# Kernel optimization log

Measured on AMD Instinct MI355X. Metric: run time of the kernel, lower is better.

## Reference

```python
import jax, jax.numpy as jnp
import numpy as np

H = 64  # hidden size


def _gru_cell(x, h, Wih, Whh, bih, bhh):
    """PyTorch-convention GRU cell. x:[B,in], h:[B,H]. Gate order: r, z, n."""
    gi = x @ Wih.T + bih              # [B, 3H]
    gh = h @ Whh.T + bhh              # [B, 3H]
    ir, iz, in_ = jnp.split(gi, 3, axis=-1)
    hr, hz, hn = jnp.split(gh, 3, axis=-1)
    r = jax.nn.sigmoid(ir + hr)
    z = jax.nn.sigmoid(iz + hz)
    n = jnp.tanh(in_ + r * hn)
    return (1.0 - z) * n + z * h


def setup_inputs() -> dict:
    key = jax.random.key(0)
    B, T, NIN = 4096, 256, 6
    ks = jax.random.split(key, 24)

    def w(k, shape, fan):
        return (jax.random.normal(k, shape, jnp.float32) / np.sqrt(fan).astype(np.float32))

    inp = {"x": jax.random.normal(ks[0], (B, T, NIN), jnp.float32)}
    # encoder layer 0 (input 6) and layer 1 (input 64)
    inp["enc_Wih0"] = w(ks[1], (3 * H, NIN), H)
    inp["enc_Whh0"] = w(ks[2], (3 * H, H), H)
    inp["enc_bih0"] = w(ks[3], (3 * H,), H)
    inp["enc_bhh0"] = w(ks[4], (3 * H,), H)
    inp["enc_Wih1"] = w(ks[5], (3 * H, H), H)
    inp["enc_Whh1"] = w(ks[6], (3 * H, H), H)
    inp["enc_bih1"] = w(ks[7], (3 * H,), H)
    inp["enc_bhh1"] = w(ks[8], (3 * H,), H)
    # decoder layer 0 (input 1) and layer 1 (input 64)
    inp["dec_Wih0"] = w(ks[9], (3 * H, 1), H)
    inp["dec_Whh0"] = w(ks[10], (3 * H, H), H)
    inp["dec_bih0"] = w(ks[11], (3 * H,), H)
    inp["dec_bhh0"] = w(ks[12], (3 * H,), H)
    inp["dec_Wih1"] = w(ks[13], (3 * H, H), H)
    inp["dec_Whh1"] = w(ks[14], (3 * H, H), H)
    inp["dec_bih1"] = w(ks[15], (3 * H,), H)
    inp["dec_bhh1"] = w(ks[16], (3 * H,), H)
    # output head
    inp["out_W"] = w(ks[17], (1, H), H)
    inp["out_b"] = w(ks[18], (1,), H)
    inp["target_len"] = 180
    return inp


def reference(x, enc_Wih0, enc_Whh0, enc_bih0, enc_bhh0,
              enc_Wih1, enc_Whh1, enc_bih1, enc_bhh1,
              dec_Wih0, dec_Whh0, dec_bih0, dec_bhh0,
              dec_Wih1, dec_Whh1, dec_bih1, dec_bhh1,
              out_W, out_b, target_len):
    B = x.shape[0]
    dtype = x.dtype

    # ---- encoder: 2-layer GRU over x, return final hidden per layer ----
    seq = jnp.swapaxes(x, 0, 1)  # [T, B, 6] time-major
    enc_layers = [(enc_Wih0, enc_Whh0, enc_bih0, enc_bhh0),
                  (enc_Wih1, enc_Whh1, enc_bih1, enc_bhh1)]
    h_finals = []
    for (Wih, Whh, bih, bhh) in enc_layers:
        def step(h, xt, Wih=Wih, Whh=Whh, bih=bih, bhh=bhh):
            hn = _gru_cell(xt, h, Wih, Whh, bih, bhh)
            return hn, hn
        h_last, seq = jax.lax.scan(step, jnp.zeros((B, H), dtype), seq)
        h_finals.append(h_last)

    def dec_step(carry, _):
        h0, h1, prev = carry
        h0 = _gru_cell(prev, h0, dec_Wih0, dec_Whh0, dec_bih0, dec_bhh0)
        h1 = _gru_cell(h0, h1, dec_Wih1, dec_Whh1, dec_bih1, dec_bhh1)
        cv = h1 @ out_W.T + out_b  # [B, 1]
        return (h0, h1, cv), cv

    prev0 = jnp.zeros((B, 1), dtype)
    _, outs = jax.lax.scan(dec_step, (h_finals[0], h_finals[1], prev0),
                           None, length=target_len)
    return jnp.swapaxes(outs, 0, 1)  # [B, target_len, 1]
```

## Files before the change

kernel.cpp:

```cpp
#include <hip/hip_runtime.h>
#include <cstdint>

typedef _Float16 half8 __attribute__((ext_vector_type(8)));
typedef __attribute__((ext_vector_type(4))) float floatx4;

#define TSEQ 256
#define TDEC 180
#define NIN  6
#define GROWS 16
#define NBLK (4096 / GROWS)
#define NSL 4
#define RS0 104
#define RS1 72
#define L2E 1.4426950408889634f

__device__ __forceinline__ floatx4 mfma16(half8 a, half8 b, floatx4 c) {
  return __builtin_amdgcn_mfma_f32_16x16x32_f16(a, b, c, 0, 0, 0);
}

__device__ __forceinline__ void sigm2pair(float vr, float vz, float& gr, float& gz) {
  const float d1 = 1.0f + __builtin_amdgcn_exp2f(-vr);
  const float d2 = 1.0f + __builtin_amdgcn_exp2f(-vz);
  const float rp = __builtin_amdgcn_rcpf(d1 * d2);
  gr = rp * d2;
  gz = rp * d1;
}
__device__ __forceinline__ float tanh2(float v) {
  return fmaf(2.0f, __builtin_amdgcn_rcpf(1.0f + __builtin_amdgcn_exp2f(-v)), -1.0f);
}

__device__ __forceinline__ half8 ldh8(const _Float16* p) { return *(const half8*)p; }

#define PASS2_I3(F0, F1, r, z, g, W, QR, QZ, QG) do {                   \
  r = mfma16(F0, W[0][0], QR); z = mfma16(F0, W[1][0], QZ); g = mfma16(F0, W[2][0], QG); \
  r = mfma16(F1, W[0][1], r);  z = mfma16(F1, W[1][1], z);  g = mfma16(F1, W[2][1], g);  \
} while (0)

#define PASS2_A2I1(F0, F1, r, z, g, W, QG) do {                         \
  r = mfma16(F0, W[0][0], r); z = mfma16(F0, W[1][0], z); g = mfma16(F0, W[2][0], QG); \
  r = mfma16(F1, W[0][1], r); z = mfma16(F1, W[1][1], z); g = mfma16(F1, W[2][1], g);  \
} while (0)

#define PASS1_A2I1(F0, r, z, g, W, QG) do {                             \
  r = mfma16(F0, W[0][0], r); z = mfma16(F0, W[1][0], z); g = mfma16(F0, W[2][0], QG); \
} while (0)

#define SYNC() do {                                         \
  asm volatile("s_waitcnt lgkmcnt(0)" ::: "memory");        \
  __builtin_amdgcn_s_barrier();                             \
  asm volatile("" ::: "memory");                            \
} while (0)

__global__ void __launch_bounds__(512, 2)
gru_persist(const float* __restrict__ x,
            const float* __restrict__ eWih0, const float* __restrict__ eWhh0,
            const float* __restrict__ ebih0, const float* __restrict__ ebhh0,
            const float* __restrict__ eWih1, const float* __restrict__ eWhh1,
            const float* __restrict__ ebih1, const float* __restrict__ ebhh1,
            const float* __restrict__ dWih0, const float* __restrict__ dWhh0,
            const float* __restrict__ dbih0, const float* __restrict__ dbhh0,
            const float* __restrict__ dWih1, const float* __restrict__ dWhh1,
            const float* __restrict__ dbih1, const float* __restrict__ dbhh1,
            const float* __restrict__ outW, const float* __restrict__ outB,
            float* __restrict__ out)
{
  __shared__ __align__(16) _Float16 s0[NSL][16][RS0];
  __shared__ __align__(16) _Float16 s1[NSL][16][RS1];

  const int tid  = threadIdx.x;
  const bool isA = tid < 256;
  const int wvL  = (tid >> 6) & 3;
  const int lane = tid & 63;
  const int c    = lane & 15;
  const int q    = lane >> 4;
  const int u    = wvL * 16 + c;
  const long base = (long)blockIdx.x * GROWS;

  for (int i = tid; i < NSL * 16 * RS0; i += 512) ((uint16_t*)s0)[i] = 0;
  for (int i = tid; i < NSL * 16 * RS1; i += 512) ((uint16_t*)s1)[i] = 0;
  if (tid < GROWS * NIN) {
    int m = tid / 6, i2 = tid - m * 6;
    s0[0][m][64 + i2] = (_Float16)x[(base + m) * (TSEQ * NIN) + i2];
  }

  half8 W1[3][2], W2[3][2];
  half8 W1d[3][2], W2d[3][2];
  float hr[4] = {0, 0, 0, 0};
  const float SC[3] = {L2E, L2E, 2.0f * L2E};

  auto loadW64 = [&](const float* W, half8 (&D)[3][2]) {
    #pragma unroll
    for (int s = 0; s < 3; s++) {
      const int n = (s * 4 + wvL) * 16 + c;
      #pragma unroll
      for (int kt = 0; kt < 2; kt++) {
        const int k0 = kt * 32 + q * 8;
        #pragma unroll
        for (int j = 0; j < 8; j++) D[s][kt][j] = (_Float16)(SC[s] * W[n * 64 + k0 + j]);
      }
    }
  };

  const float ob = outB[0];
  float cR, cZ, c3, c4;
  float dR, dZ, d3, d4;
  float bR0 = 0, bZ0 = 0, b30 = 0, b40 = 0;
  float wk[2][8];
  if (isA) {
    loadW64(eWhh0, W1);
    #pragma unroll
    for (int s = 0; s < 3; s++) {
      const int n = (s * 4 + wvL) * 16 + c;
      #pragma unroll
      for (int kt = 0; kt < 2; kt++)
        #pragma unroll
        for (int j = 0; j < 8; j++) {
          float v = (kt == 0 && q == 0 && j < NIN) ? SC[s] * eWih0[n * NIN + j] : 0.0f;
          W2[s][kt][j] = (_Float16)v;
        }
    }
    loadW64(dWhh0, W1d);
    #pragma unroll
    for (int s = 0; s < 3; s++) {
      const int n = (s * 4 + wvL) * 16 + c;
      const float wd = SC[s] * dWih0[n];
      #pragma unroll
      for (int kt = 0; kt < 2; kt++) {
        const int k0 = kt * 32 + q * 8;
        #pragma unroll
        for (int j = 0; j < 8; j++) W2d[s][kt][j] = (_Float16)(wd * outW[k0 + j]);
      }
    }
    cR = L2E * (ebih0[u] + ebhh0[u]);
    cZ = L2E * (ebih0[64 + u] + ebhh0[64 + u]);
    c3 = 2.0f * L2E * ebhh0[128 + u];
    c4 = 2.0f * L2E * ebih0[128 + u];
    bR0 = L2E * (dbih0[u] + dbhh0[u]);
    bZ0 = L2E * (dbih0[64 + u] + dbhh0[64 + u]);
    b30 = 2.0f * L2E * dbhh0[128 + u];
    b40 = 2.0f * L2E * dbih0[128 + u];
    dR = bR0 + L2E * (dWih0[u] * ob);
    dZ = bZ0 + L2E * (dWih0[64 + u] * ob);
    d3 = b30;
    d4 = b40 + 2.0f * L2E * (dWih0[128 + u] * ob);
  } else {
    loadW64(eWih1, W1); loadW64(eWhh1, W2);
    loadW64(dWih1, W1d); loadW64(dWhh1, W2d);
    cR = L2E * (ebih1[u] + ebhh1[u]);
    cZ = L2E * (ebih1[64 + u] + ebhh1[64 + u]);
    c3 = 2.0f * L2E * ebih1[128 + u];
    c4 = 2.0f * L2E * ebhh1[128 + u];
    dR = L2E * (dbih1[u] + dbhh1[u]);
    dZ = L2E * (dbih1[64 + u] + dbhh1[64 + u]);
    d3 = 2.0f * L2E * dbih1[128 + u];
    d4 = 2.0f * L2E * dbhh1[128 + u];
    #pragma unroll
    for (int kt = 0; kt < 2; kt++)
      #pragma unroll
      for (int j = 0; j < 8; j++) wk[kt][j] = outW[kt * 32 + q * 8 + j];
  }
  __syncthreads();

  if (isA) {
    floatx4 QR = {cR, cR, cR, cR}, QZ = {cZ, cZ, cZ, cZ};
    floatx4 Q3 = {c3, c3, c3, c3}, Q4 = {c4, c4, c4, c4};
    const bool doX = (lane < 24);
    const float *px0 = nullptr;
    int xo0 = 0;
    float xa0 = 0.f, xb0 = 0.f;
    if (doX) {
      int s_ = wvL * 24 + lane;
      int m0 = s_ / 6, i0 = s_ - m0 * 6;
      px0 = x + (base + m0) * (TSEQ * NIN) + i0;
      xo0 = m0 * RS0 + 64 + i0;
      xa0 = px0[NIN];
      xb0 = px0[2 * NIN];
    }
    for (int k = 0; k < TSEQ; k += 4) {
      #pragma unroll
      for (int h4 = 0; h4 < 4; h4++) {
        const int i_ = k + h4, p = h4, pn = (h4 + 1) & 3;
        const half8 a0 = ldh8(&s0[p][c][q * 8]);
        const half8 a1 = ldh8(&s0[p][c][32 + q * 8]);
        const half8 xf = ldh8(&s0[p][c][64 + q * 8]);
        floatx4 aR, aZ, a3, a4;
        PASS2_I3(a0, a1, aR, aZ, a3, W1, QR, QZ, Q3);
        PASS1_A2I1(xf, aR, aZ, a4, W2, Q4);
        if (doX && i_ + 1 < TSEQ) {
          ((_Float16*)s0[pn])[xo0] = (_Float16)xa0;
          xa0 = xb0;
          if (i_ + 3 < TSEQ) xb0 = px0[(i_ + 3) * NIN];
        }
        #pragma unroll
        for (int r4 = 0; r4 < 4; r4++) {
          float gr, gz;
          sigm2pair(aR[r4], aZ[r4], gr, gz);
          const float nn = tanh2(a4[r4] + gr * a3[r4]);
          const float hn = nn + gz * (hr[r4] - nn);
          hr[r4] = hn;
          s0[pn][q * 4 + r4][u] = (_Float16)hn;
        }
        SYNC();
      }
    }
    {
      const half8 a0 = ldh8(&s0[0][c][q * 8]);
      const half8 a1 = ldh8(&s0[0][c][32 + q * 8]);
      const floatx4 TR = {bR0, bR0, bR0, bR0}, TZ = {bZ0, bZ0, bZ0, bZ0};
      const floatx4 T3 = {b30, b30, b30, b30};
      floatx4 aR, aZ, a3;
      floatx4 a4 = {b40, b40, b40, b40};
      PASS2_I3(a0, a1, aR, aZ, a3, W1d, TR, TZ, T3);
      #pragma unroll
      for (int r4 = 0; r4 < 4; r4++) {
        float gr, gz;
        sigm2pair(aR[r4], aZ[r4], gr, gz);
        const float nn = tanh2(a4[r4] + gr * a3[r4]);
        const float hn = nn + gz * (hr[r4] - nn);
        hr[r4] = hn;
        s0[1][q * 4 + r4][u] = (_Float16)hn;
      }
      SYNC();
    }
    QR = (floatx4){dR, dR, dR, dR}; QZ = (floatx4){dZ, dZ, dZ, dZ};
    Q3 = (floatx4){d3, d3, d3, d3}; Q4 = (floatx4){d4, d4, d4, d4};
    for (int i_ = TSEQ + 1; i_ < TSEQ + TDEC; i_++) {
      const int p = i_ & 3, pn = (i_ + 1) & 3;
      const half8 a0 = ldh8(&s0[p][c][q * 8]);
      const half8 a1 = ldh8(&s0[p][c][32 + q * 8]);
      floatx4 aR, aZ, a3, a4;
      PASS2_I3(a0, a1, aR, aZ, a3, W1d, QR, QZ, Q3);
      SYNC();
      const half8 b0 = ldh8(&s1[p][c][q * 8]);
      const half8 b1 = ldh8(&s1[p][c][32 + q * 8]);
      PASS2_A2I1(b0, b1, aR, aZ, a4, W2d, Q4);
      #pragma unroll
      for (int r4 = 0; r4 < 4; r4++) {
        float gr, gz;
        sigm2pair(aR[r4], aZ[r4], gr, gz);
        const float nn = tanh2(a4[r4] + gr * a3[r4]);
        const float hn = nn + gz * (hr[r4] - nn);
        hr[r4] = hn;
        s0[pn][q * 4 + r4][u] = (_Float16)hn;
      }
      SYNC();
    }
    SYNC();
  } else {
    floatx4 QR = {cR, cR, cR, cR}, QZ = {cZ, cZ, cZ, cZ};
    floatx4 Q3 = {c3, c3, c3, c3}, Q4 = {c4, c4, c4, c4};
    for (int k = 0; k < TSEQ; k += 4) {
      #pragma unroll
      for (int h4 = 0; h4 < 4; h4++) {
        const int kk = k + h4;
        if (kk > 0) {
          const int p = (h4 + 3) & 3, pn = h4;
          const half8 f0 = ldh8(&s1[p][c][q * 8]);
          const half8 f1 = ldh8(&s1[p][c][32 + q * 8]);
          floatx4 aR, aZ, a3, a4;
          PASS2_I3(f0, f1, aR, aZ, a4, W2, QR, QZ, Q4);
          const half8 g0 = ldh8(&s0[pn][c][q * 8]);
          const half8 g1 = ldh8(&s0[pn][c][32 + q * 8]);
          PASS2_A2I1(g0, g1, aR, aZ, a3, W1, Q3);
          #pragma unroll
          for (int r4 = 0; r4 < 4; r4++) {
            float gr, gz;
            sigm2pair(aR[r4], aZ[r4], gr, gz);
            const float nn = tanh2(a3[r4] + gr * a4[r4]);
            const float hn = nn + gz * (hr[r4] - nn);
            hr[r4] = hn;
            s1[pn][q * 4 + r4][u] = (_Float16)hn;
          }
        }
        SYNC();
      }
    }
    {
      const half8 f0 = ldh8(&s1[3][c][q * 8]);
      const half8 f1 = ldh8(&s1[3][c][32 + q * 8]);
      floatx4 aR, aZ, a3, a4;
      PASS2_I3(f0, f1, aR, aZ, a4, W2, QR, QZ, Q4);
      const half8 g0 = ldh8(&s0[0][c][q * 8]);
      const half8 g1 = ldh8(&s0[0][c][32 + q * 8]);
      PASS2_A2I1(g0, g1, aR, aZ, a3, W1, Q3);
      #pragma unroll
      for (int r4 = 0; r4 < 4; r4++) {
        float gr, gz;
        sigm2pair(aR[r4], aZ[r4], gr, gz);
        const float nn = tanh2(a3[r4] + gr * a4[r4]);
        const float hn = nn + gz * (hr[r4] - nn);
        hr[r4] = hn;
        s1[0][q * 4 + r4][u] = (_Float16)hn;
      }
      SYNC();
    }
    QR = (floatx4){dR, dR, dR, dR}; QZ = (floatx4){dZ, dZ, dZ, dZ};
    Q3 = (floatx4){d3, d3, d3, d3}; Q4 = (floatx4){d4, d4, d4, d4};
    {
      const half8 f0 = ldh8(&s1[0][c][q * 8]);
      const half8 f1 = ldh8(&s1[0][c][32 + q * 8]);
      floatx4 aR, aZ, a3, a4;
      PASS2_I3(f0, f1, aR, aZ, a4, W2d, QR, QZ, Q4);
      const half8 g0 = ldh8(&s0[1][c][q * 8]);
      const half8 g1 = ldh8(&s0[1][c][32 + q * 8]);
      PASS2_A2I1(g0, g1, aR, aZ, a3, W1d, Q3);
      #pragma unroll
      for (int r4 = 0; r4 < 4; r4++) {
        float gr, gz;
        sigm2pair(aR[r4], aZ[r4], gr, gz);
        const float nn = tanh2(a3[r4] + gr * a4[r4]);
        const float hn = nn + gz * (hr[r4] - nn);
        hr[r4] = hn;
        s1[1][q * 4 + r4][u] = (_Float16)hn;
      }
      SYNC();
    }
    for (int i_ = TSEQ + 1; i_ < TSEQ + TDEC; i_++) {
      const int p = i_ & 3, pn = (i_ + 1) & 3;
      const half8 f0 = ldh8(&s1[p][c][q * 8]);
      const half8 f1 = ldh8(&s1[p][c][32 + q * 8]);
      floatx4 aR, aZ, a3, a4;
      PASS2_I3(f0, f1, aR, aZ, a4, W2d, QR, QZ, Q4);
      if (wvL == 0) {
        float cv = 0.0f;
        #pragma unroll
        for (int j = 0; j < 8; j++) {
          cv = fmaf((float)f0[j], wk[0][j], cv);
          cv = fmaf((float)f1[j], wk[1][j], cv);
        }
        cv += __shfl_xor(cv, 16);
        cv += __shfl_xor(cv, 32);
        if (lane < 16) out[(base + lane) * TDEC + (i_ - TSEQ - 1)] = cv + ob;
      }
      SYNC();
      const half8 g0 = ldh8(&s0[pn][c][q * 8]);
      const half8 g1 = ldh8(&s0[pn][c][32 + q * 8]);
      PASS2_A2I1(g0, g1, aR, aZ, a3, W1d, Q3);
      #pragma unroll
      for (int r4 = 0; r4 < 4; r4++) {
        float gr, gz;
        sigm2pair(aR[r4], aZ[r4], gr, gz);
        const float nn = tanh2(a3[r4] + gr * a4[r4]);
        const float hn = nn + gz * (hr[r4] - nn);
        hr[r4] = hn;
        s1[pn][q * 4 + r4][u] = (_Float16)hn;
      }
      SYNC();
    }
    if (wvL == 0) {
      const half8 f0 = ldh8(&s1[0][c][q * 8]);
      const half8 f1 = ldh8(&s1[0][c][32 + q * 8]);
      float cv = 0.0f;
      #pragma unroll
      for (int j = 0; j < 8; j++) {
        cv = fmaf((float)f0[j], wk[0][j], cv);
        cv = fmaf((float)f1[j], wk[1][j], cv);
      }
      cv += __shfl_xor(cv, 16);
      cv += __shfl_xor(cv, 32);
      if (lane < 16) out[(base + lane) * TDEC + (TDEC - 1)] = cv + ob;
    }
  }
}

extern "C" void kernel_launch(void* const* d_in, const int* in_sizes, int n_in,
                              void* d_out, int out_size, void* d_ws, size_t ws_size,
                              hipStream_t stream) {
  (void)in_sizes; (void)n_in; (void)d_ws; (void)ws_size; (void)out_size;
  const float* x     = (const float*)d_in[0];
  const float* eWih0 = (const float*)d_in[1];
  const float* eWhh0 = (const float*)d_in[2];
  const float* ebih0 = (const float*)d_in[3];
  const float* ebhh0 = (const float*)d_in[4];
  const float* eWih1 = (const float*)d_in[5];
  const float* eWhh1 = (const float*)d_in[6];
  const float* ebih1 = (const float*)d_in[7];
  const float* ebhh1 = (const float*)d_in[8];
  const float* dWih0 = (const float*)d_in[9];
  const float* dWhh0 = (const float*)d_in[10];
  const float* dbih0 = (const float*)d_in[11];
  const float* dbhh0 = (const float*)d_in[12];
  const float* dWih1 = (const float*)d_in[13];
  const float* dWhh1 = (const float*)d_in[14];
  const float* dbih1 = (const float*)d_in[15];
  const float* dbhh1 = (const float*)d_in[16];
  const float* outW  = (const float*)d_in[17];
  const float* outB  = (const float*)d_in[18];
  hipLaunchKernelGGL(gru_persist, dim3(NBLK), dim3(512), 0, stream,
                     x, eWih0, eWhh0, ebih0, ebhh0, eWih1, eWhh1, ebih1, ebhh1,
                     dWih0, dWhh0, dbih0, dbhh0, dWih1, dWhh1, dbih1, dbhh1,
                     outW, outB, (float*)d_out);
}
```

Measured before the change: 362.9 us.

## Merge two GRU layer wave groups into single 256-thread block per row tile

Replaces the 512-thread block, where the first 256 threads ran layer 0 and the second 256 ran layer 1, with 256 threads that each compute both layers in the same step. The encoder pipelines layer 1 for step i-1 alongside layer 0 for step i inside one barrier interval. Decoder weights are loaded after the encoder finishes to limit register pressure. Launch bounds change to (256,1); this halves the threads working on each tile and roughly doubles the serial MFMA and transcendental work per wave, in exchange for less cross-group synchronisation.

```diff
diff --git a/kernel.cpp b/kernel.cpp
--- a/kernel.cpp
+++ b/kernel.cpp
@@ -14,6 +14,7 @@
 #define RS1 72
 #define L2E 1.4426950408889634f
 
+
 __device__ __forceinline__ floatx4 mfma16(half8 a, half8 b, floatx4 c) {
   return __builtin_amdgcn_mfma_f32_16x16x32_f16(a, b, c, 0, 0, 0);
 }
@@ -30,6 +31,7 @@
 }
 
 __device__ __forceinline__ half8 ldh8(const _Float16* p) { return *(const half8*)p; }
+__device__ __forceinline__ floatx4 sp4(float v) { return (floatx4){v, v, v, v}; }
 
 #define PASS2_I3(F0, F1, r, z, g, W, QR, QZ, QG) do {                   \
   r = mfma16(F0, W[0][0], QR); z = mfma16(F0, W[1][0], QZ); g = mfma16(F0, W[2][0], QG); \
@@ -41,8 +43,8 @@
   r = mfma16(F1, W[0][1], r); z = mfma16(F1, W[1][1], z); g = mfma16(F1, W[2][1], g);  \
 } while (0)
 
-#define PASS1_A2I1(F0, r, z, g, W, QG) do {                             \
-  r = mfma16(F0, W[0][0], r); z = mfma16(F0, W[1][0], z); g = mfma16(F0, W[2][0], QG); \
+#define PASS1_I1(F0, r, z, g, W3, QG) do {                              \
+  r = mfma16(F0, W3[0], r); z = mfma16(F0, W3[1], z); g = mfma16(F0, W3[2], QG); \
 } while (0)
 
 #define SYNC() do {                                         \
@@ -51,7 +53,7 @@
   asm volatile("" ::: "memory");                            \
 } while (0)
 
-__global__ void __launch_bounds__(512, 2)
+__global__ void __launch_bounds__(256, 1)
 gru_persist(const float* __restrict__ x,
             const float* __restrict__ eWih0, const float* __restrict__ eWhh0,
             const float* __restrict__ ebih0, const float* __restrict__ ebhh0,
@@ -68,24 +70,26 @@
   __shared__ __align__(16) _Float16 s1[NSL][16][RS1];
 
   const int tid  = threadIdx.x;
-  const bool isA = tid < 256;
-  const int wvL  = (tid >> 6) & 3;
+  const int wvL  = tid >> 6;
   const int lane = tid & 63;
   const int c    = lane & 15;
   const int q    = lane >> 4;
   const int u    = wvL * 16 + c;
   const long base = (long)blockIdx.x * GROWS;
 
-  for (int i = tid; i < NSL * 16 * RS0; i += 512) ((uint16_t*)s0)[i] = 0;
-  for (int i = tid; i < NSL * 16 * RS1; i += 512) ((uint16_t*)s1)[i] = 0;
+  for (int i = tid; i < NSL * 16 * RS0; i += 256) ((uint16_t*)s0)[i] = 0;
+  for (int i = tid; i < NSL * 16 * RS1; i += 256) ((uint16_t*)s1)[i] = 0;
   if (tid < GROWS * NIN) {
     int m = tid / 6, i2 = tid - m * 6;
     s0[0][m][64 + i2] = (_Float16)x[(base + m) * (TSEQ * NIN) + i2];
   }
 
-  half8 W1[3][2], W2[3][2];
-  half8 W1d[3][2], W2d[3][2];
-  float hr[4] = {0, 0, 0, 0};
+  half8 W1[3][2];
+  half8 W2e[3];
+  half8 W1B[3][2];
+  half8 W2B[3][2];
+  float hr0[4] = {0, 0, 0, 0};
+  float hr1[4] = {0, 0, 0, 0};
   const float SC[3] = {L2E, L2E, 2.0f * L2E};
 
   auto loadW64 = [&](const float* W, half8 (&D)[3][2]) {
@@ -101,265 +105,241 @@
     }
   };
 
+  loadW64(eWhh0, W1);
+  #pragma unroll
+  for (int s = 0; s < 3; s++) {
+    const int n = (s * 4 + wvL) * 16 + c;
+    #pragma unroll
+    for (int j = 0; j < 8; j++) {
+      float v = (q == 0 && j < NIN) ? SC[s] * eWih0[n * NIN + j] : 0.0f;
+      W2e[s][j] = (_Float16)v;
+    }
+  }
+  loadW64(eWih1, W1B);
+  loadW64(eWhh1, W2B);
+
   const float ob = outB[0];
-  float cR, cZ, c3, c4;
-  float dR, dZ, d3, d4;
-  float bR0 = 0, bZ0 = 0, b30 = 0, b40 = 0;
   float wk[2][8];
-  if (isA) {
-    loadW64(eWhh0, W1);
-    #pragma unroll
-    for (int s = 0; s < 3; s++) {
-      const int n = (s * 4 + wvL) * 16 + c;
-      #pragma unroll
-      for (int kt = 0; kt < 2; kt++)
-        #pragma unroll
-        for (int j = 0; j < 8; j++) {
-          float v = (kt == 0 && q == 0 && j < NIN) ? SC[s] * eWih0[n * NIN + j] : 0.0f;
-          W2[s][kt][j] = (_Float16)v;
-        }
-    }
-    loadW64(dWhh0, W1d);
-    #pragma unroll
-    for (int s = 0; s < 3; s++) {
-      const int n = (s * 4 + wvL) * 16 + c;
-      const float wd = SC[s] * dWih0[n];
-      #pragma unroll
-      for (int kt = 0; kt < 2; kt++) {
-        const int k0 = kt * 32 + q * 8;
-        #pragma unroll
-        for (int j = 0; j < 8; j++) W2d[s][kt][j] = (_Float16)(wd * outW[k0 + j]);
-      }
-    }
-    cR = L2E * (ebih0[u] + ebhh0[u]);
-    cZ = L2E * (ebih0[64 + u] + ebhh0[64 + u]);
-    c3 = 2.0f * L2E * ebhh0[128 + u];
-    c4 = 2.0f * L2E * ebih0[128 + u];
-    bR0 = L2E * (dbih0[u] + dbhh0[u]);
-    bZ0 = L2E * (dbih0[64 + u] + dbhh0[64 + u]);
-    b30 = 2.0f * L2E * dbhh0[128 + u];
-    b40 = 2.0f * L2E * dbih0[128 + u];
-    dR = bR0 + L2E * (dWih0[u] * ob);
-    dZ = bZ0 + L2E * (dWih0[64 + u] * ob);
-    d3 = b30;
-    d4 = b40 + 2.0f * L2E * (dWih0[128 + u] * ob);
-  } else {
-    loadW64(eWih1, W1); loadW64(eWhh1, W2);
-    loadW64(dWih1, W1d); loadW64(dWhh1, W2d);
-    cR = L2E * (ebih1[u] + ebhh1[u]);
-    cZ = L2E * (ebih1[64 + u] + ebhh1[64 + u]);
-    c3 = 2.0f * L2E * ebih1[128 + u];
-    c4 = 2.0f * L2E * ebhh1[128 + u];
-    dR = L2E * (dbih1[u] + dbhh1[u]);
-    dZ = L2E * (dbih1[64 + u] + dbhh1[64 + u]);
-    d3 = 2.0f * L2E * dbih1[128 + u];
-    d4 = 2.0f * L2E * dbhh1[128 + u];
-    #pragma unroll
-    for (int kt = 0; kt < 2; kt++)
-      #pragma unroll
-      for (int j = 0; j < 8; j++) wk[kt][j] = outW[kt * 32 + q * 8 + j];
-  }
+  #pragma unroll
+  for (int kt = 0; kt < 2; kt++)
+    #pragma unroll
+    for (int j = 0; j < 8; j++) wk[kt][j] = outW[kt * 32 + q * 8 + j];
+
+  const floatx4 QR0 = sp4(L2E * (ebih0[u] + ebhh0[u]));
+  const floatx4 QZ0 = sp4(L2E * (ebih0[64 + u] + ebhh0[64 + u]));
+  const floatx4 Q30 = sp4(2.0f * L2E * ebhh0[128 + u]);
+  const floatx4 Q40 = sp4(2.0f * L2E * ebih0[128 + u]);
+  const floatx4 QR1 = sp4(L2E * (ebih1[u] + ebhh1[u]));
+  const floatx4 QZ1 = sp4(L2E * (ebih1[64 + u] + ebhh1[64 + u]));
+  const floatx4 Q31 = sp4(2.0f * L2E * ebih1[128 + u]);
+  const floatx4 Q41 = sp4(2.0f * L2E * ebhh1[128 + u]);
+
   __syncthreads();
 
-  if (isA) {
-    floatx4 QR = {cR, cR, cR, cR}, QZ = {cZ, cZ, cZ, cZ};
-    floatx4 Q3 = {c3, c3, c3, c3}, Q4 = {c4, c4, c4, c4};
-    const bool doX = (lane < 24);
-    const float *px0 = nullptr;
-    int xo0 = 0;
-    float xa0 = 0.f, xb0 = 0.f;
-    if (doX) {
-      int s_ = wvL * 24 + lane;
-      int m0 = s_ / 6, i0 = s_ - m0 * 6;
-      px0 = x + (base + m0) * (TSEQ * NIN) + i0;
-      xo0 = m0 * RS0 + 64 + i0;
-      xa0 = px0[NIN];
-      xb0 = px0[2 * NIN];
-    }
-    for (int k = 0; k < TSEQ; k += 4) {
-      #pragma unroll
-      for (int h4 = 0; h4 < 4; h4++) {
-        const int i_ = k + h4, p = h4, pn = (h4 + 1) & 3;
-        const half8 a0 = ldh8(&s0[p][c][q * 8]);
-        const half8 a1 = ldh8(&s0[p][c][32 + q * 8]);
-        const half8 xf = ldh8(&s0[p][c][64 + q * 8]);
-        floatx4 aR, aZ, a3, a4;
-        PASS2_I3(a0, a1, aR, aZ, a3, W1, QR, QZ, Q3);
-        PASS1_A2I1(xf, aR, aZ, a4, W2, Q4);
-        if (doX && i_ + 1 < TSEQ) {
-          ((_Float16*)s0[pn])[xo0] = (_Float16)xa0;
-          xa0 = xb0;
-          if (i_ + 3 < TSEQ) xb0 = px0[(i_ + 3) * NIN];
-        }
-        #pragma unroll
-        for (int r4 = 0; r4 < 4; r4++) {
-          float gr, gz;
-          sigm2pair(aR[r4], aZ[r4], gr, gz);
-          const float nn = tanh2(a4[r4] + gr * a3[r4]);
-          const float hn = nn + gz * (hr[r4] - nn);
-          hr[r4] = hn;
-          s0[pn][q * 4 + r4][u] = (_Float16)hn;
-        }
-        SYNC();
-      }
-    }
-    {
-      const half8 a0 = ldh8(&s0[0][c][q * 8]);
-      const half8 a1 = ldh8(&s0[0][c][32 + q * 8]);
-      const floatx4 TR = {bR0, bR0, bR0, bR0}, TZ = {bZ0, bZ0, bZ0, bZ0};
-      const floatx4 T3 = {b30, b30, b30, b30};
-      floatx4 aR, aZ, a3;
-      floatx4 a4 = {b40, b40, b40, b40};
-      PASS2_I3(a0, a1, aR, aZ, a3, W1d, TR, TZ, T3);
+  const bool doX = (lane < 24);
+  const float *px0 = nullptr;
+  int xo0 = 0;
+  float xa0 = 0.f, xb0 = 0.f;
+  if (doX) {
+    int s_ = wvL * 24 + lane;
+    int m0 = s_ / 6, i0 = s_ - m0 * 6;
+    px0 = x + (base + m0) * (TSEQ * NIN) + i0;
+    xo0 = m0 * RS0 + 64 + i0;
+    xa0 = px0[NIN];
+    xb0 = px0[2 * NIN];
+  }
+
+  for (int k = 0; k < TSEQ; k += 4) {
+    #pragma unroll
+    for (int h4 = 0; h4 < 4; h4++) {
+      const int i_ = k + h4;
+      const int p  = h4;
+      const int pn = (h4 + 1) & 3;
+      const int pm = (h4 + 3) & 3;
+      const half8 a0 = ldh8(&s0[p][c][q * 8]);
+      const half8 a1 = ldh8(&s0[p][c][32 + q * 8]);
+      const half8 xf = ldh8(&s0[p][c][64 + q * 8]);
+      floatx4 aR, aZ, a3, a4;
+      PASS2_I3(a0, a1, aR, aZ, a3, W1, QR0, QZ0, Q30);
+      PASS1_I1(xf, aR, aZ, a4, W2e, Q40);
+      floatx4 fR, fZ, fG, fI;
+      if (i_ > 0) {
+        const half8 f0 = ldh8(&s1[pm][c][q * 8]);
+        const half8 f1 = ldh8(&s1[pm][c][32 + q * 8]);
+        PASS2_I3(f0, f1, fR, fZ, fG, W2B, QR1, QZ1, Q41);
+        PASS2_A2I1(a0, a1, fR, fZ, fI, W1B, Q31);
+      }
+      if (doX && i_ + 1 < TSEQ) {
+        ((_Float16*)s0[pn])[xo0] = (_Float16)xa0;
+        xa0 = xb0;
+        if (i_ + 3 < TSEQ) xb0 = px0[(i_ + 3) * NIN];
+      }
       #pragma unroll
       for (int r4 = 0; r4 < 4; r4++) {
         float gr, gz;
         sigm2pair(aR[r4], aZ[r4], gr, gz);
         const float nn = tanh2(a4[r4] + gr * a3[r4]);
-        const float hn = nn + gz * (hr[r4] - nn);
-        hr[r4] = hn;
-        s0[1][q * 4 + r4][u] = (_Float16)hn;
+        const float hn = nn + gz * (hr0[r4] - nn);
+        hr0[r4] = hn;
+        s0[pn][q * 4 + r4][u] = (_Float16)hn;
+      }
+      if (i_ > 0) {
+        #pragma unroll
+        for (int r4 = 0; r4 < 4; r4++) {
+          float gr, gz;
+          sigm2pair(fR[r4], fZ[r4], gr, gz);
+          const float nn = tanh2(fI[r4] + gr * fG[r4]);
+          const float hn = nn + gz * (hr1[r4] - nn);
+          hr1[r4] = hn;
+          s1[p][q * 4 + r4][u] = (_Float16)hn;
+        }
       }
       SYNC();
     }
-    QR = (floatx4){dR, dR, dR, dR}; QZ = (floatx4){dZ, dZ, dZ, dZ};
-    Q3 = (floatx4){d3, d3, d3, d3}; Q4 = (floatx4){d4, d4, d4, d4};
-    for (int i_ = TSEQ + 1; i_ < TSEQ + TDEC; i_++) {
-      const int p = i_ & 3, pn = (i_ + 1) & 3;
-      const half8 a0 = ldh8(&s0[p][c][q * 8]);
-      const half8 a1 = ldh8(&s0[p][c][32 + q * 8]);
-      floatx4 aR, aZ, a3, a4;
-      PASS2_I3(a0, a1, aR, aZ, a3, W1d, QR, QZ, Q3);
-      SYNC();
-      const half8 b0 = ldh8(&s1[p][c][q * 8]);
-      const half8 b1 = ldh8(&s1[p][c][32 + q * 8]);
-      PASS2_A2I1(b0, b1, aR, aZ, a4, W2d, Q4);
+  }
+  {
+    const half8 g0 = ldh8(&s0[0][c][q * 8]);
+    const half8 g1 = ldh8(&s0[0][c][32 + q * 8]);
+    const half8 f0 = ldh8(&s1[3][c][q * 8]);
+    const half8 f1 = ldh8(&s1[3][c][32 + q * 8]);
+    floatx4 fR, fZ, fG, fI;
+    PASS2_I3(f0, f1, fR, fZ, fG, W2B, QR1, QZ1, Q41);
+    PASS2_A2I1(g0, g1, fR, fZ, fI, W1B, Q31);
+    #pragma unroll
+    for (int r4 = 0; r4 < 4; r4++) {
+      float gr, gz;
+      sigm2pair(fR[r4], fZ[r4], gr, gz);
+      const float nn = tanh2(fI[r4] + gr * fG[r4]);
+      const float hn = nn + gz * (hr1[r4] - nn);
+      hr1[r4] = hn;
+      s1[0][q * 4 + r4][u] = (_Float16)hn;
+    }
+    SYNC();
+  }
+
+  half8 W1d[3][2], W2d[3][2];
+  half8 W1dB[3][2], W2dB[3][2];
+  loadW64(dWhh0, W1d);
+  #pragma unroll
+  for (int s = 0; s < 3; s++) {
+    const int n = (s * 4 + wvL) * 16 + c;
+    const float wd = SC[s] * dWih0[n];
+    #pragma unroll
+    for (int kt = 0; kt < 2; kt++) {
+      const int k0 = kt * 32 + q * 8;
       #pragma unroll
-      for (int r4 = 0; r4 < 4; r4++) {
-        float gr, gz;
-        sigm2pair(aR[r4], aZ[r4], gr, gz);
-        const float nn = tanh2(a4[r4] + gr * a3[r4]);
-        const float hn = nn + gz * (hr[r4] - nn);
-        hr[r4] = hn;
-        s0[pn][q * 4 + r4][u] = (_Float16)hn;
-      }
-      SYNC();
-    }
-    SYNC();
-  } else {
-    floatx4 QR = {cR, cR, cR, cR}, QZ = {cZ, cZ, cZ, cZ};
-    floatx4 Q3 = {c3, c3, c3, c3}, Q4 = {c4, c4, c4, c4};
-    for (int k = 0; k < TSEQ; k += 4) {
-      #pragma unroll
-      for (int h4 = 0; h4 < 4; h4++) {
-        const int kk = k + h4;
-        if (kk > 0) {
-          const int p = (h4 + 3) & 3, pn = h4;
-          const half8 f0 = ldh8(&s1[p][c][q * 8]);
-          const half8 f1 = ldh8(&s1[p][c][32 + q * 8]);
-          floatx4 aR, aZ, a3, a4;
-          PASS2_I3(f0, f1, aR, aZ, a4, W2, QR, QZ, Q4);
-          const half8 g0 = ldh8(&s0[pn][c][q * 8]);
-          const half8 g1 = ldh8(&s0[pn][c][32 + q * 8]);
-          PASS2_A2I1(g0, g1, aR, aZ, a3, W1, Q3);
-          #pragma unroll
-          for (int r4 = 0; r4 < 4; r4++) {
-            float gr, gz;
-            sigm2pair(aR[r4], aZ[r4], gr, gz);
-            const float nn = tanh2(a3[r4] + gr * a4[r4]);
-            const float hn = nn + gz * (hr[r4] - nn);
-            hr[r4] = hn;
-            s1[pn][q * 4 + r4][u] = (_Float16)hn;
-          }
-        }
-        SYNC();
-      }
-    }
-    {
-      const half8 f0 = ldh8(&s1[3][c][q * 8]);
-      const half8 f1 = ldh8(&s1[3][c][32 + q * 8]);
-      floatx4 aR, aZ, a3, a4;
-      PASS2_I3(f0, f1, aR, aZ, a4, W2, QR, QZ, Q4);
-      const half8 g0 = ldh8(&s0[0][c][q * 8]);
-      const half8 g1 = ldh8(&s0[0][c][32 + q * 8]);
-      PASS2_A2I1(g0, g1, aR, aZ, a3, W1, Q3);
-      #pragma unroll
-      for (int r4 = 0; r4 < 4; r4++) {
-        float gr, gz;
-        sigm2pair(aR[r4], aZ[r4], gr, gz);
-        const float nn = tanh2(a3[r4] + gr * a4[r4]);
-        const float hn = nn + gz * (hr[r4] - nn);
-        hr[r4] = hn;
-        s1[0][q * 4 + r4][u] = (_Float16)hn;
-      }
-      SYNC();
-    }
-    QR = (floatx4){dR, dR, dR, dR}; QZ = (floatx4){dZ, dZ, dZ, dZ};
-    Q3 = (floatx4){d3, d3, d3, d3}; Q4 = (floatx4){d4, d4, d4, d4};
-    {
-      const half8 f0 = ldh8(&s1[0][c][q * 8]);
-      const half8 f1 = ldh8(&s1[0][c][32 + q * 8]);
-      floatx4 aR, aZ, a3, a4;
-      PASS2_I3(f0, f1, aR, aZ, a4, W2d, QR, QZ, Q4);
-      const half8 g0 = ldh8(&s0[1][c][q * 8]);
-      const half8 g1 = ldh8(&s0[1][c][32 + q * 8]);
-      PASS2_A2I1(g0, g1, aR, aZ, a3, W1d, Q3);
-      #pragma unroll
-      for (int r4 = 0; r4 < 4; r4++) {
-        float gr, gz;
-        sigm2pair(aR[r4], aZ[r4], gr, gz);
-        const float nn = tanh2(a3[r4] + gr * a4[r4]);
-        const float hn = nn + gz * (hr[r4] - nn);
-        hr[r4] = hn;
-        s1[1][q * 4 + r4][u] = (_Float16)hn;
-      }
-      SYNC();
-    }
-    for (int i_ = TSEQ + 1; i_ < TSEQ + TDEC; i_++) {
-      const int p = i_ & 3, pn = (i_ + 1) & 3;
-      const half8 f0 = ldh8(&s1[p][c][q * 8]);
-      const half8 f1 = ldh8(&s1[p][c][32 + q * 8]);
-      floatx4 aR, aZ, a3, a4;
-      PASS2_I3(f0, f1, aR, aZ, a4, W2d, QR, QZ, Q4);
-      if (wvL == 0) {
-        float cv = 0.0f;
-        #pragma unroll
-        for (int j = 0; j < 8; j++) {
-          cv = fmaf((float)f0[j], wk[0][j], cv);
-          cv = fmaf((float)f1[j], wk[1][j], cv);
-        }
-        cv += __shfl_xor(cv, 16);
-        cv += __shfl_xor(cv, 32);
-        if (lane < 16) out[(base + lane) * TDEC + (i_ - TSEQ - 1)] = cv + ob;
-      }
-      SYNC();
-      const half8 g0 = ldh8(&s0[pn][c][q * 8]);
-      const half8 g1 = ldh8(&s0[pn][c][32 + q * 8]);
-      PASS2_A2I1(g0, g1, aR, aZ, a3, W1d, Q3);
-      #pragma unroll
-      for (int r4 = 0; r4 < 4; r4++) {
-        float gr, gz;
-        sigm2pair(aR[r4], aZ[r4], gr, gz);
-        const float nn = tanh2(a3[r4] + gr * a4[r4]);
-        const float hn = nn + gz * (hr[r4] - nn);
-        hr[r4] = hn;
-        s1[pn][q * 4 + r4][u] = (_Float16)hn;
-      }
-      SYNC();
-    }
+      for (int j = 0; j < 8; j++) W2d[s][kt][j] = (_Float16)(wd * outW[k0 + j]);
+    }
+  }
+  loadW64(dWih1, W1dB);
+  loadW64(dWhh1, W2dB);
+  const float bR0 = L2E * (dbih0[u] + dbhh0[u]);
+  const float bZ0 = L2E * (dbih0[64 + u] + dbhh0[64 + u]);
+  const float b30 = 2.0f * L2E * dbhh0[128 + u];
+  const float b40 = 2.0f * L2E * dbih0[128 + u];
+  const floatx4 QRd = sp4(bR0 + L2E * (dWih0[u] * ob));
+  const floatx4 QZd = sp4(bZ0 + L2E * (dWih0[64 + u] * ob));
+  const floatx4 Q3d = sp4(b30);
+  const floatx4 Q4d = sp4(b40 + 2.0f * L2E * (dWih0[128 + u] * ob));
+  const floatx4 QR1d = sp4(L2E * (dbih1[u] + dbhh1[u]));
+  const floatx4 QZ1d = sp4(L2E * (dbih1[64 + u] + dbhh1[64 + u]));
+  const floatx4 Q31d = sp4(2.0f * L2E * dbih1[128 + u]);
+  const floatx4 Q41d = sp4(2.0f * L2E * dbhh1[128 + u]);
+
+  {
+    const half8 a0 = ldh8(&s0[0][c][q * 8]);
+    const half8 a1 = ldh8(&s0[0][c][32 + q * 8]);
+    const floatx4 TR = sp4(bR0), TZ = sp4(bZ0), T3 = sp4(b30);
+    floatx4 aR, aZ, a3;
+    PASS2_I3(a0, a1, aR, aZ, a3, W1d, TR, TZ, T3);
+    #pragma unroll
+    for (int r4 = 0; r4 < 4; r4++) {
+      float gr, gz;
+      sigm2pair(aR[r4], aZ[r4], gr, gz);
+      const float nn = tanh2(b40 + gr * a3[r4]);
+      const float hn = nn + gz * (hr0[r4] - nn);
+      hr0[r4] = hn;
+      s0[1][q * 4 + r4][u] = (_Float16)hn;
+    }
+    SYNC();
+  }
+  {
+    const half8 f0 = ldh8(&s1[0][c][q * 8]);
+    const half8 f1 = ldh8(&s1[0][c][32 + q * 8]);
+    const half8 g0 = ldh8(&s0[1][c][q * 8]);
+    const half8 g1 = ldh8(&s0[1][c][32 + q * 8]);
+    floatx4 fR, fZ, fG, fI;
+    PASS2_I3(f0, f1, fR, fZ, fG, W2dB, QR1d, QZ1d, Q41d);
+    PASS2_A2I1(g0, g1, fR, fZ, fI, W1dB, Q31d);
+    #pragma unroll
+    for (int r4 = 0; r4 < 4; r4++) {
+      float gr, gz;
+      sigm2pair(fR[r4], fZ[r4], gr, gz);
+      const float nn = tanh2(fI[r4] + gr * fG[r4]);
+      const float hn = nn + gz * (hr1[r4] - nn);
+      hr1[r4] = hn;
+      s1[1][q * 4 + r4][u] = (_Float16)hn;
+    }
+    SYNC();
+  }
+  for (int i_ = TSEQ + 1; i_ < TSEQ + TDEC; i_++) {
+    const int p = i_ & 3, pn = (i_ + 1) & 3;
+    const half8 a0 = ldh8(&s0[p][c][q * 8]);
+    const half8 a1 = ldh8(&s0[p][c][32 + q * 8]);
+    const half8 b0 = ldh8(&s1[p][c][q * 8]);
+    const half8 b1 = ldh8(&s1[p][c][32 + q * 8]);
+    floatx4 aR, aZ, a3, a4;
+    PASS2_I3(a0, a1, aR, aZ, a3, W1d, QRd, QZd, Q3d);
+    PASS2_A2I1(b0, b1, aR, aZ, a4, W2d, Q4d);
     if (wvL == 0) {
-      const half8 f0 = ldh8(&s1[0][c][q * 8]);
-      const half8 f1 = ldh8(&s1[0][c][32 + q * 8]);
       float cv = 0.0f;
       #pragma unroll
       for (int j = 0; j < 8; j++) {
-        cv = fmaf((float)f0[j], wk[0][j], cv);
-        cv = fmaf((float)f1[j], wk[1][j], cv);
+        cv = fmaf((float)b0[j], wk[0][j], cv);
+        cv = fmaf((float)b1[j], wk[1][j], cv);
       }
       cv += __shfl_xor(cv, 16);
       cv += __shfl_xor(cv, 32);
-      if (lane < 16) out[(base + lane) * TDEC + (TDEC - 1)] = cv + ob;
-    }
+      if (lane < 16) out[(base + lane) * TDEC + (i_ - TSEQ - 1)] = cv + ob;
+    }
+    #pragma unroll
+    for (int r4 = 0; r4 < 4; r4++) {
+      float gr, gz;
+      sigm2pair(aR[r4], aZ[r4], gr, gz);
+      const float nn = tanh2(a4[r4] + gr * a3[r4]);
+      const float hn = nn + gz * (hr0[r4] - nn);
+      hr0[r4] = hn;
+      s0[pn][q * 4 + r4][u] = (_Float16)hn;
+    }
+    SYNC();
+    const half8 g0 = ldh8(&s0[pn][c][q * 8]);
+    const half8 g1 = ldh8(&s0[pn][c][32 + q * 8]);
+    floatx4 fR, fZ, fG, fI;
+    PASS2_I3(b0, b1, fR, fZ, fG, W2dB, QR1d, QZ1d, Q41d);
+    PASS2_A2I1(g0, g1, fR, fZ, fI, W1dB, Q31d);
+    #pragma unroll
+    for (int r4 = 0; r4 < 4; r4++) {
+      float gr, gz;
+      sigm2pair(fR[r4], fZ[r4], gr, gz);
+      const float nn = tanh2(fI[r4] + gr * fG[r4]);
+      const float hn = nn + gz * (hr1[r4] - nn);
+      hr1[r4] = hn;
+      s1[pn][q * 4 + r4][u] = (_Float16)hn;
+    }
+    SYNC();
+  }
+  if (wvL == 0) {
+    const half8 f0 = ldh8(&s1[0][c][q * 8]);
+    const half8 f1 = ldh8(&s1[0][c][32 + q * 8]);
+    float cv = 0.0f;
+    #pragma unroll
+    for (int j = 0; j < 8; j++) {
+      cv = fmaf((float)f0[j], wk[0][j], cv);
+      cv = fmaf((float)f1[j], wk[1][j], cv);
+    }
+    cv += __shfl_xor(cv, 16);
+    cv += __shfl_xor(cv, 32);
+    if (lane < 16) out[(base + lane) * TDEC + (TDEC - 1)] = cv + ob;
   }
 }
 
@@ -386,7 +366,7 @@
   const float* dbhh1 = (const float*)d_in[16];
   const float* outW  = (const float*)d_in[17];
   const float* outB  = (const float*)d_in[18];
-  hipLaunchKernelGGL(gru_persist, dim3(NBLK), dim3(512), 0, stream,
+  hipLaunchKernelGGL(gru_persist, dim3(NBLK), dim3(256), 0, stream,
                      x, eWih0, eWhh0, ebih0, ebhh0, eWih1, eWhh1, ebih1, ebhh1,
                      dWih0, dWhh0, dbih0, dbhh0, dWih1, dWhh1, dbih1, dbhh1,
                      outW, outB, (float*)d_out);
```

Measured after the change: 421.4 us. 1.16x slower.

## Transpose MFMA operands so each lane writes four contiguous hidden units

Applied to the files above, without the earlier changes.

Swaps the A/B operands of the MFMA calls so the output tile is transposed. Each lane now holds four consecutive hidden units of one batch row and stores them with a single 4-half vector write instead of four scalar LDS stores. The bias vectors become per-element floatx4 values, and the gate nonlinearities are rewritten in packed float2 form, sharing one reciprocal between the two tanh values. The encoder input projection also drops its unused zero weight half. These changes aim to cut LDS store instructions and VALU work on the serial recurrence path, at the cost of more bias registers.

```diff
diff --git a/kernel.cpp b/kernel.cpp
--- a/kernel.cpp
+++ b/kernel.cpp
@@ -2,7 +2,9 @@
 #include <cstdint>
 
 typedef _Float16 half8 __attribute__((ext_vector_type(8)));
+typedef _Float16 half4v __attribute__((ext_vector_type(4)));
 typedef __attribute__((ext_vector_type(4))) float floatx4;
+typedef __attribute__((ext_vector_type(2))) float float2v;
 
 #define TSEQ 256
 #define TDEC 180
@@ -18,31 +20,20 @@
   return __builtin_amdgcn_mfma_f32_16x16x32_f16(a, b, c, 0, 0, 0);
 }
 
-__device__ __forceinline__ void sigm2pair(float vr, float vz, float& gr, float& gz) {
-  const float d1 = 1.0f + __builtin_amdgcn_exp2f(-vr);
-  const float d2 = 1.0f + __builtin_amdgcn_exp2f(-vz);
-  const float rp = __builtin_amdgcn_rcpf(d1 * d2);
-  gr = rp * d2;
-  gz = rp * d1;
-}
-__device__ __forceinline__ float tanh2(float v) {
-  return fmaf(2.0f, __builtin_amdgcn_rcpf(1.0f + __builtin_amdgcn_exp2f(-v)), -1.0f);
-}
-
 __device__ __forceinline__ half8 ldh8(const _Float16* p) { return *(const half8*)p; }
 
 #define PASS2_I3(F0, F1, r, z, g, W, QR, QZ, QG) do {                   \
-  r = mfma16(F0, W[0][0], QR); z = mfma16(F0, W[1][0], QZ); g = mfma16(F0, W[2][0], QG); \
-  r = mfma16(F1, W[0][1], r);  z = mfma16(F1, W[1][1], z);  g = mfma16(F1, W[2][1], g);  \
+  r = mfma16(W[0][0], F0, QR); z = mfma16(W[1][0], F0, QZ); g = mfma16(W[2][0], F0, QG); \
+  r = mfma16(W[0][1], F1, r);  z = mfma16(W[1][1], F1, z);  g = mfma16(W[2][1], F1, g);  \
 } while (0)
 
 #define PASS2_A2I1(F0, F1, r, z, g, W, QG) do {                         \
-  r = mfma16(F0, W[0][0], r); z = mfma16(F0, W[1][0], z); g = mfma16(F0, W[2][0], QG); \
-  r = mfma16(F1, W[0][1], r); z = mfma16(F1, W[1][1], z); g = mfma16(F1, W[2][1], g);  \
+  r = mfma16(W[0][0], F0, r); z = mfma16(W[1][0], F0, z); g = mfma16(W[2][0], F0, QG); \
+  r = mfma16(W[0][1], F1, r); z = mfma16(W[1][1], F1, z); g = mfma16(W[2][1], F1, g);  \
 } while (0)
 
-#define PASS1_A2I1(F0, r, z, g, W, QG) do {                             \
-  r = mfma16(F0, W[0][0], r); z = mfma16(F0, W[1][0], z); g = mfma16(F0, W[2][0], QG); \
+#define PASS1_I1(F0, r, z, g, W3, QG) do {                              \
+  r = mfma16(W3[0], F0, r); z = mfma16(W3[1], F0, z); g = mfma16(W3[2], F0, QG); \
 } while (0)
 
 #define SYNC() do {                                         \
@@ -74,6 +65,7 @@
   const int c    = lane & 15;
   const int q    = lane >> 4;
   const int u    = wvL * 16 + c;
+  const int ub   = wvL * 16 + q * 4;
   const long base = (long)blockIdx.x * GROWS;
 
   for (int i = tid; i < NSL * 16 * RS0; i += 512) ((uint16_t*)s0)[i] = 0;
@@ -84,6 +76,7 @@
   }
 
   half8 W1[3][2], W2[3][2];
+  half8 W2e[3];
   half8 W1d[3][2], W2d[3][2];
   float hr[4] = {0, 0, 0, 0};
   const float SC[3] = {L2E, L2E, 2.0f * L2E};
@@ -101,10 +94,40 @@
     }
   };
 
+  auto NLIN = [&](const floatx4 R, const floatx4 Z, const floatx4 GIN, const floatx4 GHN,
+                  _Float16* dst) {
+    half4v hv;
+    #pragma unroll
+    for (int pr = 0; pr < 2; pr++) {
+      const int e = pr * 2;
+      float2v er, ez;
+      er.x = __builtin_amdgcn_exp2f(-R[e]);   er.y = __builtin_amdgcn_exp2f(-R[e + 1]);
+      ez.x = __builtin_amdgcn_exp2f(-Z[e]);   ez.y = __builtin_amdgcn_exp2f(-Z[e + 1]);
+      const float2v Dr = 1.0f + er, Dz = 1.0f + ez;
+      const float2v P  = Dr * Dz;
+      float2v rp;
+      rp.x = __builtin_amdgcn_rcpf(P.x);      rp.y = __builtin_amdgcn_rcpf(P.y);
+      const float2v gr = rp * Dz, gz = rp * Dr;
+      const float2v gin = {GIN[e], GIN[e + 1]}, ghn = {GHN[e], GHN[e + 1]};
+      const float2v vn = gin + gr * ghn;
+      float2v en;
+      en.x = __builtin_amdgcn_exp2f(-vn.x);   en.y = __builtin_amdgcn_exp2f(-vn.y);
+      const float2v Dn = 1.0f + en;
+      const float rpn = __builtin_amdgcn_rcpf(Dn.x * Dn.y);
+      const float2v dsw = {Dn.y, Dn.x};
+      const float2v nn = (2.0f * rpn) * dsw - 1.0f;
+      const float2v hold = {hr[e], hr[e + 1]};
+      const float2v hn = nn + gz * (hold - nn);
+      hr[e] = hn.x; hr[e + 1] = hn.y;
+      hv[e] = (_Float16)hn.x; hv[e + 1] = (_Float16)hn.y;
+    }
+    *(half4v*)dst = hv;
+  };
+
   const float ob = outB[0];
-  float cR, cZ, c3, c4;
-  float dR, dZ, d3, d4;
-  float bR0 = 0, bZ0 = 0, b30 = 0, b40 = 0;
+  floatx4 QR, QZ, Q3, Q4;
+  floatx4 DRv, DZv, D3v, D4v;
+  floatx4 TRv, TZv, T3v, T4v;
   float wk[2][8];
   if (isA) {
     loadW64(eWhh0, W1);
@@ -112,12 +135,10 @@
     for (int s = 0; s < 3; s++) {
       const int n = (s * 4 + wvL) * 16 + c;
       #pragma unroll
-      for (int kt = 0; kt < 2; kt++)
-        #pragma unroll
-        for (int j = 0; j < 8; j++) {
-          float v = (kt == 0 && q == 0 && j < NIN) ? SC[s] * eWih0[n * NIN + j] : 0.0f;
-          W2[s][kt][j] = (_Float16)v;
-        }
+      for (int j = 0; j < 8; j++) {
+        float v = (q == 0 && j < NIN) ? SC[s] * eWih0[n * NIN + j] : 0.0f;
+        W2e[s][j] = (_Float16)v;
+      }
     }
     loadW64(dWhh0, W1d);
     #pragma unroll
@@ -131,29 +152,37 @@
         for (int j = 0; j < 8; j++) W2d[s][kt][j] = (_Float16)(wd * outW[k0 + j]);
       }
     }
-    cR = L2E * (ebih0[u] + ebhh0[u]);
-    cZ = L2E * (ebih0[64 + u] + ebhh0[64 + u]);
-    c3 = 2.0f * L2E * ebhh0[128 + u];
-    c4 = 2.0f * L2E * ebih0[128 + u];
-    bR0 = L2E * (dbih0[u] + dbhh0[u]);
-    bZ0 = L2E * (dbih0[64 + u] + dbhh0[64 + u]);
-    b30 = 2.0f * L2E * dbhh0[128 + u];
-    b40 = 2.0f * L2E * dbih0[128 + u];
-    dR = bR0 + L2E * (dWih0[u] * ob);
-    dZ = bZ0 + L2E * (dWih0[64 + u] * ob);
-    d3 = b30;
-    d4 = b40 + 2.0f * L2E * (dWih0[128 + u] * ob);
+    #pragma unroll
+    for (int r = 0; r < 4; r++) {
+      const int g = ub + r;
+      QR[r] = L2E * (ebih0[g] + ebhh0[g]);
+      QZ[r] = L2E * (ebih0[64 + g] + ebhh0[64 + g]);
+      Q3[r] = 2.0f * L2E * ebhh0[128 + g];
+      Q4[r] = 2.0f * L2E * ebih0[128 + g];
+      TRv[r] = L2E * (dbih0[g] + dbhh0[g]);
+      TZv[r] = L2E * (dbih0[64 + g] + dbhh0[64 + g]);
+      T3v[r] = 2.0f * L2E * dbhh0[128 + g];
+      T4v[r] = 2.0f * L2E * dbih0[128 + g];
+      DRv[r] = TRv[r] + L2E * (dWih0[g] * ob);
+      DZv[r] = TZv[r] + L2E * (dWih0[64 + g] * ob);
+      D3v[r] = T3v[r];
+      D4v[r] = T4v[r] + 2.0f * L2E * (dWih0[128 + g] * ob);
+    }
   } else {
     loadW64(eWih1, W1); loadW64(eWhh1, W2);
     loadW64(dWih1, W1d); loadW64(dWhh1, W2d);
-    cR = L2E * (ebih1[u] + ebhh1[u]);
-    cZ = L2E * (ebih1[64 + u] + ebhh1[64 + u]);
-    c3 = 2.0f * L2E * ebih1[128 + u];
-    c4 = 2.0f * L2E * ebhh1[128 + u];
-    dR = L2E * (dbih1[u] + dbhh1[u]);
-    dZ = L2E * (dbih1[64 + u] + dbhh1[64 + u]);
-    d3 = 2.0f * L2E * dbih1[128 + u];
-    d4 = 2.0f * L2E * dbhh1[128 + u];
+    #pragma unroll
+    for (int r = 0; r < 4; r++) {
+      const int g = ub + r;
+      QR[r] = L2E * (ebih1[g] + ebhh1[g]);
+      QZ[r] = L2E * (ebih1[64 + g] + ebhh1[64 + g]);
+      Q3[r] = 2.0f * L2E * ebih1[128 + g];
+      Q4[r] = 2.0f * L2E * ebhh1[128 + g];
+      DRv[r] = L2E * (dbih1[g] + dbhh1[g]);
+      DZv[r] = L2E * (dbih1[64 + g] + dbhh1[64 + g]);
+      D3v[r] = 2.0f * L2E * dbih1[128 + g];
+      D4v[r] = 2.0f * L2E * dbhh1[128 + g];
+    }
     #pragma unroll
     for (int kt = 0; kt < 2; kt++)
       #pragma unroll
@@ -162,8 +191,6 @@
   __syncthreads();
 
   if (isA) {
-    floatx4 QR = {cR, cR, cR, cR}, QZ = {cZ, cZ, cZ, cZ};
-    floatx4 Q3 = {c3, c3, c3, c3}, Q4 = {c4, c4, c4, c4};
     const bool doX = (lane < 24);
     const float *px0 = nullptr;
     int xo0 = 0;
@@ -183,72 +210,45 @@
         const half8 a0 = ldh8(&s0[p][c][q * 8]);
         const half8 a1 = ldh8(&s0[p][c][32 + q * 8]);
         const half8 xf = ldh8(&s0[p][c][64 + q * 8]);
-        floatx4 aR, aZ, a3, a4;
-        PASS2_I3(a0, a1, aR, aZ, a3, W1, QR, QZ, Q3);
-        PASS1_A2I1(xf, aR, aZ, a4, W2, Q4);
+        floatx4 aR = QR, aZ = QZ, a3 = Q3, a4 = Q4;
+        {
+          floatx4 tR, tZ, tG;
+          PASS2_I3(a0, a1, tR, tZ, tG, W1, aR, aZ, a3);
+          aR = tR; aZ = tZ; a3 = tG;
+        }
+        PASS1_I1(xf, aR, aZ, a4, W2e, a4);
         if (doX && i_ + 1 < TSEQ) {
           ((_Float16*)s0[pn])[xo0] = (_Float16)xa0;
           xa0 = xb0;
           if (i_ + 3 < TSEQ) xb0 = px0[(i_ + 3) * NIN];
         }
-        #pragma unroll
-        for (int r4 = 0; r4 < 4; r4++) {
-          float gr, gz;
-          sigm2pair(aR[r4], aZ[r4], gr, gz);
-          const float nn = tanh2(a4[r4] + gr * a3[r4]);
-          const float hn = nn + gz * (hr[r4] - nn);
-          hr[r4] = hn;
-          s0[pn][q * 4 + r4][u] = (_Float16)hn;
-        }
+        NLIN(aR, aZ, a4, a3, &s0[pn][c][ub]);
         SYNC();
       }
     }
     {
       const half8 a0 = ldh8(&s0[0][c][q * 8]);
       const half8 a1 = ldh8(&s0[0][c][32 + q * 8]);
-      const floatx4 TR = {bR0, bR0, bR0, bR0}, TZ = {bZ0, bZ0, bZ0, bZ0};
-      const floatx4 T3 = {b30, b30, b30, b30};
       floatx4 aR, aZ, a3;
-      floatx4 a4 = {b40, b40, b40, b40};
-      PASS2_I3(a0, a1, aR, aZ, a3, W1d, TR, TZ, T3);
-      #pragma unroll
-      for (int r4 = 0; r4 < 4; r4++) {
-        float gr, gz;
-        sigm2pair(aR[r4], aZ[r4], gr, gz);
-        const float nn = tanh2(a4[r4] + gr * a3[r4]);
-        const float hn = nn + gz * (hr[r4] - nn);
-        hr[r4] = hn;
-        s0[1][q * 4 + r4][u] = (_Float16)hn;
-      }
-      SYNC();
-    }
-    QR = (floatx4){dR, dR, dR, dR}; QZ = (floatx4){dZ, dZ, dZ, dZ};
-    Q3 = (floatx4){d3, d3, d3, d3}; Q4 = (floatx4){d4, d4, d4, d4};
+      PASS2_I3(a0, a1, aR, aZ, a3, W1d, TRv, TZv, T3v);
+      NLIN(aR, aZ, T4v, a3, &s0[1][c][ub]);
+      SYNC();
+    }
     for (int i_ = TSEQ + 1; i_ < TSEQ + TDEC; i_++) {
       const int p = i_ & 3, pn = (i_ + 1) & 3;
       const half8 a0 = ldh8(&s0[p][c][q * 8]);
       const half8 a1 = ldh8(&s0[p][c][32 + q * 8]);
       floatx4 aR, aZ, a3, a4;
-      PASS2_I3(a0, a1, aR, aZ, a3, W1d, QR, QZ, Q3);
+      PASS2_I3(a0, a1, aR, aZ, a3, W1d, DRv, DZv, D3v);
       SYNC();
       const half8 b0 = ldh8(&s1[p][c][q * 8]);
       const half8 b1 = ldh8(&s1[p][c][32 + q * 8]);
-      PASS2_A2I1(b0, b1, aR, aZ, a4, W2d, Q4);
-      #pragma unroll
-      for (int r4 = 0; r4 < 4; r4++) {
-        float gr, gz;
-        sigm2pair(aR[r4], aZ[r4], gr, gz);
-        const float nn = tanh2(a4[r4] + gr * a3[r4]);
-        const float hn = nn + gz * (hr[r4] - nn);
-        hr[r4] = hn;
-        s0[pn][q * 4 + r4][u] = (_Float16)hn;
-      }
+      PASS2_A2I1(b0, b1, aR, aZ, a4, W2d, D4v);
+      NLIN(aR, aZ, a4, a3, &s0[pn][c][ub]);
       SYNC();
     }
     SYNC();
   } else {
-    floatx4 QR = {cR, cR, cR, cR}, QZ = {cZ, cZ, cZ, cZ};
-    floatx4 Q3 = {c3, c3, c3, c3}, Q4 = {c4, c4, c4, c4};
     for (int k = 0; k < TSEQ; k += 4) {
       #pragma unroll
       for (int h4 = 0; h4 < 4; h4++) {
@@ -262,15 +262,7 @@
           const half8 g0 = ldh8(&s0[pn][c][q * 8]);
           const half8 g1 = ldh8(&s0[pn][c][32 + q * 8]);
           PASS2_A2I1(g0, g1, aR, aZ, a3, W1, Q3);
-          #pragma unroll
-          for (int r4 = 0; r4 < 4; r4++) {
-            float gr, gz;
-            sigm2pair(aR[r4], aZ[r4], gr, gz);
-            const float nn = tanh2(a3[r4] + gr * a4[r4]);
-            const float hn = nn + gz * (hr[r4] - nn);
-            hr[r4] = hn;
-            s1[pn][q * 4 + r4][u] = (_Float16)hn;
-          }
+          NLIN(aR, aZ, a3, a4, &s1[pn][c][ub]);
         }
         SYNC();
       }
@@ -283,36 +275,18 @@
       const half8 g0 = ldh8(&s0[0][c][q * 8]);
       const half8 g1 = ldh8(&s0[0][c][32 + q * 8]);
       PASS2_A2I1(g0, g1, aR, aZ, a3, W1, Q3);
-      #pragma unroll
-      for (int r4 = 0; r4 < 4; r4++) {
-        float gr, gz;
-        sigm2pair(aR[r4], aZ[r4], gr, gz);
-        const float nn = tanh2(a3[r4] + gr * a4[r4]);
-        const float hn = nn + gz * (hr[r4] - nn);
-        hr[r4] = hn;
-        s1[0][q * 4 + r4][u] = (_Float16)hn;
-      }
-      SYNC();
-    }
-    QR = (floatx4){dR, dR, dR, dR}; QZ = (floatx4){dZ, dZ, dZ, dZ};
-    Q3 = (floatx4){d3, d3, d3, d3}; Q4 = (floatx4){d4, d4, d4, d4};
+      NLIN(aR, aZ, a3, a4, &s1[0][c][ub]);
+      SYNC();
+    }
     {
       const half8 f0 = ldh8(&s1[0][c][q * 8]);
       const half8 f1 = ldh8(&s1[0][c][32 + q * 8]);
       floatx4 aR, aZ, a3, a4;
-      PASS2_I3(f0, f1, aR, aZ, a4, W2d, QR, QZ, Q4);
+      PASS2_I3(f0, f1, aR, aZ, a4, W2d, DRv, DZv, D4v);
       const half8 g0 = ldh8(&s0[1][c][q * 8]);
       const half8 g1 = ldh8(&s0[1][c][32 + q * 8]);
-      PASS2_A2I1(g0, g1, aR, aZ, a3, W1d, Q3);
-      #pragma unroll
-      for (int r4 = 0; r4 < 4; r4++) {
-        float gr, gz;
-        sigm2pair(aR[r4], aZ[r4], gr, gz);
-        const float nn = tanh2(a3[r4] + gr * a4[r4]);
-        const float hn = nn + gz * (hr[r4] - nn);
-        hr[r4] = hn;
-        s1[1][q * 4 + r4][u] = (_Float16)hn;
-      }
+      PASS2_A2I1(g0, g1, aR, aZ, a3, W1d, D3v);
+      NLIN(aR, aZ, a3, a4, &s1[1][c][ub]);
       SYNC();
     }
     for (int i_ = TSEQ + 1; i_ < TSEQ + TDEC; i_++) {
@@ -320,7 +294,7 @@
       const half8 f0 = ldh8(&s1[p][c][q * 8]);
       const half8 f1 = ldh8(&s1[p][c][32 + q * 8]);
       floatx4 aR, aZ, a3, a4;
-      PASS2_I3(f0, f1, aR, aZ, a4, W2d, QR, QZ, Q4);
+      PASS2_I3(f0, f1, aR, aZ, a4, W2d, DRv, DZv, D4v);
       if (wvL == 0) {
         float cv = 0.0f;
         #pragma unroll
@@ -335,16 +309,8 @@
       SYNC();
       const half8 g0 = ldh8(&s0[pn][c][q * 8]);
       const half8 g1 = ldh8(&s0[pn][c][32 + q * 8]);
-      PASS2_A2I1(g0, g1, aR, aZ, a3, W1d, Q3);
-      #pragma unroll
-      for (int r4 = 0; r4 < 4; r4++) {
-        float gr, gz;
-        sigm2pair(aR[r4], aZ[r4], gr, gz);
-        const float nn = tanh2(a3[r4] + gr * a4[r4]);
-        const float hn = nn + gz * (hr[r4] - nn);
-        hr[r4] = hn;
-        s1[pn][q * 4 + r4][u] = (_Float16)hn;
-      }
+      PASS2_A2I1(g0, g1, aR, aZ, a3, W1d, D3v);
+      NLIN(aR, aZ, a3, a4, &s1[pn][c][ub]);
       SYNC();
     }
     if (wvL == 0) {
```

Result: faster. 346.8 us (-4.4%).
